# Performance work log

Hardware: AMD Instinct MI355X
Metric: run time of the kernel (lower is better)

The kernel has to match this reference:

```python
import jax, jax.numpy as jnp
import numpy as np

N_LEVELS = 8
BASE_RES = 512
FEAT = 16
N = 1_000_000


def setup_inputs() -> dict:
    key = jax.random.key(0)
    k1, k2, k3 = jax.random.split(key, 3)
    x = jax.random.uniform(k1, (N, 3), dtype=jnp.float32)  # coords in [0,1]^3
    level = jax.random.uniform(k2, (N, 1), dtype=jnp.float32) * (N_LEVELS - 1)
    # texture param: uniform(-0.01, 0.01) as in torch init
    texture = (jax.random.uniform(k3, (3, BASE_RES, BASE_RES, FEAT), dtype=jnp.float32) - 0.5) * 0.02
    return {"x": x, "level": level, "texture": texture}


def _build_mips(texture):
    """Box-filtered mip pyramid: level k has resolution BASE_RES >> k."""
    mips = [texture]
    for _ in range(N_LEVELS - 1):
        t = mips[-1]
        r = t.shape[1]
        t = t.reshape(3, r // 2, 2, r // 2, 2, FEAT).mean(axis=(2, 4))
        mips.append(t)
    return mips


def _bilinear(tex_l, uv):
    """tex_l: (3, r, r, F) [plane, v(row), u(col), feat]; uv: (3, N, 2) in [0,1]. Clamp boundary."""
    r = tex_l.shape[1]
    c = uv * r - 0.5                     # nvdiffrast texel-center convention
    i0f = jnp.floor(c)
    f = c - i0f                          # (3, N, 2) fractional part
    i0 = jnp.clip(i0f.astype(jnp.int32), 0, r - 1)
    i1 = jnp.clip(i0f.astype(jnp.int32) + 1, 0, r - 1)
    u0, v0 = i0[..., 0], i0[..., 1]
    u1, v1 = i1[..., 0], i1[..., 1]
    plane = jnp.arange(3)[:, None]       # (3, 1) broadcast against (3, N)
    t00 = tex_l[plane, v0, u0]           # (3, N, F)
    t01 = tex_l[plane, v0, u1]
    t10 = tex_l[plane, v1, u0]
    t11 = tex_l[plane, v1, u1]
    fu = f[..., 0][..., None]
    fv = f[..., 1][..., None]
    return (t00 * (1 - fu) + t01 * fu) * (1 - fv) + (t10 * (1 - fu) + t11 * fu) * fv


def reference(x, level, texture):
    n = x.shape[0]
    # plane decomposition: uv = (yz, xz, xy), last dim is (u, v)
    uv = jnp.stack([x[:, jnp.array([1, 2])],
                    x[:, jnp.array([0, 2])],
                    x[:, jnp.array([0, 1])]], axis=0)  # (3, N, 2)
    lev = jnp.clip(level[:, 0], 0.0, N_LEVELS - 1)     # (N,)
    l0f = jnp.floor(lev)
    frac = lev - l0f
    l0 = l0f.astype(jnp.int32)
    mips = _build_mips(texture)
    acc = jnp.zeros((3, n, FEAT), dtype=texture.dtype)
    for k in range(N_LEVELS):
        w = jnp.where(l0 == k, 1.0 - frac, 0.0) + jnp.where(l0 + 1 == k, frac, 0.0)  # (N,)
        acc = acc + _bilinear(mips[k], uv) * w[None, :, None]
    # (3, N, F) -> (N, 3, F) -> (N, 3F), matching permute(1,2,0,3).view(N, 3F)
    return acc.transpose(1, 0, 2).reshape(n, 3 * FEAT)
```

## Files before the change

kernel.cpp:

```cpp
#include <hip/hip_runtime.h>
#include <hip/hip_fp16.h>

#define NLEV 8
#define BASE 512

typedef _Float16 h8 __attribute__((ext_vector_type(8)));
typedef float f4v __attribute__((ext_vector_type(4)));
typedef signed char c8 __attribute__((ext_vector_type(8)));

#define QSCALE 12700.0f

__host__ __device__ __forceinline__ long qoff(int k) {
    return (k == 0) ? 0L : (12582912L + 4194304L - (4194304L >> (2 * k - 2)));
}
#define QPYR_BYTES 16776960L
#define QOFF4      16711680L
#define LDSB       65280
__host__ __device__ __forceinline__ long moff(int k) {
    return 4194304L - (4194304L >> (2 * k - 2));
}
#define MIPS_HALVES 4194048L

__global__ __launch_bounds__(256) void ds16_first(const float* __restrict__ src,
                                                  _Float16* __restrict__ dst,
                                                  signed char* __restrict__ qpyr, int r2) {
    int idx = blockIdx.x * blockDim.x + threadIdx.x;
    int total = 3 * r2 * r2 * 2;
    if (idx >= total) return;
    int g = idx & 1;
    int rest = idx >> 1;
    int u = rest % r2; rest /= r2;
    int v = rest % r2;
    int p = rest / r2;
    int rs = r2 * 2;
    const f4v* s4 = (const f4v*)src;
    long t00 = ((long)p * rs + 2 * v) * rs + 2 * u;
    long t01 = t00 + 1, t10 = t00 + rs, t11 = t10 + 1;
    f4v a0 = s4[t00 * 4 + g * 2], a1 = s4[t00 * 4 + g * 2 + 1];
    f4v b0 = s4[t01 * 4 + g * 2], b1 = s4[t01 * 4 + g * 2 + 1];
    f4v c0 = s4[t10 * 4 + g * 2], c1 = s4[t10 * 4 + g * 2 + 1];
    f4v d0 = s4[t11 * 4 + g * 2], d1 = s4[t11 * 4 + g * 2 + 1];
    h8 o;
    c8 qa, qb_, qc, qd, qo;
#pragma unroll
    for (int j = 0; j < 4; ++j) {
        float m0 = (a0[j] + b0[j] + c0[j] + d0[j]) * 0.25f;
        float m1 = (a1[j] + b1[j] + c1[j] + d1[j]) * 0.25f;
        o[j] = (_Float16)m0; o[4 + j] = (_Float16)m1;
        qo[j] = (signed char)(int)rintf(m0 * QSCALE);
        qo[4 + j] = (signed char)(int)rintf(m1 * QSCALE);
        qa[j] = (signed char)(int)rintf(a0[j] * QSCALE); qa[4 + j] = (signed char)(int)rintf(a1[j] * QSCALE);
        qb_[j] = (signed char)(int)rintf(b0[j] * QSCALE); qb_[4 + j] = (signed char)(int)rintf(b1[j] * QSCALE);
        qc[j] = (signed char)(int)rintf(c0[j] * QSCALE); qc[4 + j] = (signed char)(int)rintf(c1[j] * QSCALE);
        qd[j] = (signed char)(int)rintf(d0[j] * QSCALE); qd[4 + j] = (signed char)(int)rintf(d1[j] * QSCALE);
    }
    ((h8*)dst)[idx] = o;
    *(c8*)(qpyr + t00 * 16 + g * 8) = qa;
    *(c8*)(qpyr + t01 * 16 + g * 8) = qb_;
    *(c8*)(qpyr + t10 * 16 + g * 8) = qc;
    *(c8*)(qpyr + t11 * 16 + g * 8) = qd;
    *(c8*)(qpyr + qoff(1) + (long)idx * 8) = qo;
}

__global__ __launch_bounds__(256) void ds16(const _Float16* __restrict__ src,
                                            _Float16* __restrict__ dst,
                                            signed char* __restrict__ qlvl, int r2) {
    int idx = blockIdx.x * blockDim.x + threadIdx.x;
    int total = 3 * r2 * r2 * 2;
    if (idx >= total) return;
    int g = idx & 1;
    int rest = idx >> 1;
    int u = rest % r2; rest /= r2;
    int v = rest % r2;
    int p = rest / r2;
    int rs = r2 * 2;
    const h8* s8 = (const h8*)src;
    long t00 = ((long)p * rs + 2 * v) * rs + 2 * u;
    long t01 = t00 + 1, t10 = t00 + rs, t11 = t10 + 1;
    h8 A = s8[t00 * 2 + g], B = s8[t01 * 2 + g], C = s8[t10 * 2 + g], D = s8[t11 * 2 + g];
    h8 o;
    c8 q;
#pragma unroll
    for (int j = 0; j < 8; ++j) {
        float m = ((float)A[j] + (float)B[j] + (float)C[j] + (float)D[j]) * 0.25f;
        o[j] = (_Float16)m;
        q[j] = (signed char)(int)rintf(m * QSCALE);
    }
    ((h8*)dst)[idx] = o;
    *(c8*)(qlvl + (long)idx * 8) = q;
}

__global__ __launch_bounds__(1024, 2) void tm_sample_l(const float* __restrict__ x,
                                                       const float* __restrict__ level,
                                                       const signed char* __restrict__ qpyr,
                                                       float* __restrict__ out, int n) {
    __shared__ alignas(16) signed char lm[LDSB];
    {
        const f4v* src = (const f4v*)(qpyr + QOFF4);
        f4v* dst = (f4v*)lm;
        for (int idx = threadIdx.x; idx < LDSB / 16; idx += 1024)
            dst[idx] = src[idx];
    }
    __syncthreads();

    int fg = threadIdx.x & 1;
    int usel = (threadIdx.x >> 1) & 1;
    int pid = threadIdx.x >> 2;

    for (long base = (long)blockIdx.x * 256; base < (long)n; base += (long)gridDim.x * 256) {
        int i = (int)(base + pid);
        if (i < n) {
            float px = x[3 * i + 0];
            float py = x[3 * i + 1];
            float pz = x[3 * i + 2];
            float lev = fminf(fmaxf(level[i], 0.0f), (float)(NLEV - 1));
            float l0f = floorf(lev);
            float frac = lev - l0f;
            int l0 = (int)l0f;
            int k1 = min(l0 + 1, NLEV - 1);
            int kk[2] = {l0, k1};

            float uu[3] = {py, px, px};
            float vv[3] = {pz, pz, py};
            const float QINV = 1.0f / QSCALE;
            float lw[2] = {(1.0f - frac) * QINV, frac * QINV};

            c8 tq[12];
            float wgt[12];

#pragma unroll
            for (int s = 0; s < 2; ++s) {
                int k = kk[s];
                int r = BASE >> k;
                float rf = (float)r;
                bool in_lds = (k >= 4);
                long gbase = qoff(k);
                int lbase = (int)(gbase - QOFF4);
#pragma unroll
                for (int p = 0; p < 3; ++p) {
                    float cu = uu[p] * rf - 0.5f;
                    float cv = vv[p] * rf - 0.5f;
                    float fu0 = floorf(cu), fv0 = floorf(cv);
                    float fu = cu - fu0, fv = cv - fv0;
                    int iu0 = (int)fu0, iv0 = (int)fv0;
                    int u0 = min(max(iu0, 0), r - 1);
                    int u1 = min(max(iu0 + 1, 0), r - 1);
                    int v0 = min(max(iv0, 0), r - 1);
                    int v1 = min(max(iv0 + 1, 0), r - 1);
                    int u_ = usel ? u1 : u0;
                    float wu_ = usel ? fu : (1.0f - fu);
                    int pb = p * r * r;
                    int b0 = (pb + v0 * r + u_) * 16 + fg * 8;
                    int b1 = (pb + v1 * r + u_) * 16 + fg * 8;
                    int id = s * 6 + p * 2;
                    if (in_lds) {
                        tq[id + 0] = *(const c8*)(lm + lbase + b0);
                        tq[id + 1] = *(const c8*)(lm + lbase + b1);
                    } else {
                        tq[id + 0] = *(const c8*)(qpyr + gbase + b0);
                        tq[id + 1] = *(const c8*)(qpyr + gbase + b1);
                    }
                    wgt[id + 0] = (1.0f - fv) * wu_ * lw[s];
                    wgt[id + 1] = fv * wu_ * lw[s];
                }
            }

            float acc[3][8];
#pragma unroll
            for (int p = 0; p < 3; ++p)
#pragma unroll
                for (int j = 0; j < 8; ++j) acc[p][j] = 0.f;

#pragma unroll
            for (int s = 0; s < 2; ++s)
#pragma unroll
                for (int p = 0; p < 3; ++p) {
                    int id = s * 6 + p * 2;
                    float w0 = wgt[id + 0], w1 = wgt[id + 1];
#pragma unroll
                    for (int j = 0; j < 8; ++j)
                        acc[p][j] += (float)tq[id + 0][j] * w0 + (float)tq[id + 1][j] * w1;
                }

#pragma unroll
            for (int p = 0; p < 3; ++p)
#pragma unroll
                for (int j = 0; j < 8; ++j)
                    acc[p][j] += __shfl_xor(acc[p][j], 2, 64);

            f4v* o4 = (f4v*)out;
            long ob = (long)i * 12 + fg * 2;
            if (usel == 0) {
                f4v r0 = {acc[0][0], acc[0][1], acc[0][2], acc[0][3]};
                f4v r1 = {acc[0][4], acc[0][5], acc[0][6], acc[0][7]};
                f4v r4 = {acc[2][0], acc[2][1], acc[2][2], acc[2][3]};
                f4v r5 = {acc[2][4], acc[2][5], acc[2][6], acc[2][7]};
                o4[ob + 0] = r0;
                o4[ob + 1] = r1;
                o4[ob + 8] = r4;
                o4[ob + 9] = r5;
            } else {
                f4v r2 = {acc[1][0], acc[1][1], acc[1][2], acc[1][3]};
                f4v r3 = {acc[1][4], acc[1][5], acc[1][6], acc[1][7]};
                o4[ob + 4] = r2;
                o4[ob + 5] = r3;
            }
        }
    }
}

extern "C" void kernel_launch(void* const* d_in, const int* in_sizes, int n_in,
                              void* d_out, int out_size, void* d_ws, size_t ws_size,
                              hipStream_t stream) {
    const float* x     = (const float*)d_in[0];
    const float* level = (const float*)d_in[1];
    const float* tex   = (const float*)d_in[2];
    float* out = (float*)d_out;
    signed char* qpyr = (signed char*)d_ws;
    _Float16* wsh = (_Float16*)((char*)d_ws + QPYR_BYTES);
    int n = in_sizes[0] / 3;

    {
        int r2 = BASE >> 1;
        int total = 3 * r2 * r2 * 2;
        ds16_first<<<(total + 255) / 256, 256, 0, stream>>>(tex, wsh + moff(1), qpyr, r2);
    }
    for (int k = 2; k < NLEV; ++k) {
        int r2 = BASE >> k;
        int total = 3 * r2 * r2 * 2;
        ds16<<<(total + 255) / 256, 256, 0, stream>>>(wsh + moff(k - 1), wsh + moff(k),
                                                      qpyr + qoff(k), r2);
    }

    tm_sample_l<<<512, 1024, 0, stream>>>(x, level, qpyr, out, n);
}
```

Baseline: 141.3 us.

## Split quantized pyramid into feature-half planes and fetch texel pairs with 16-byte loads

The int8 mip pyramid is re-laid out as per-plane, per-feature-half arrays, so two horizontally adjacent texels sit next to each other in 8-byte slots. The sampler now uses two threads per point instead of four. Each thread loads both u-neighbours with a single 16-byte global load and picks the right halves at the clamped boundary, which halves the number of gather instructions and drops the cross-lane shuffle. The LDS staging of the coarse levels is removed, so every level is now read through the cache hierarchy. The twelve loads are issued together through inline asm to increase memory-level parallelism, at the cost of more registers per thread.

```diff
diff --git a/kernel.cpp b/kernel.cpp
--- a/kernel.cpp
+++ b/kernel.cpp
@@ -7,6 +7,8 @@
 typedef _Float16 h8 __attribute__((ext_vector_type(8)));
 typedef float f4v __attribute__((ext_vector_type(4)));
 typedef signed char c8 __attribute__((ext_vector_type(8)));
+typedef signed char c16 __attribute__((ext_vector_type(16)));
+typedef int  i4v __attribute__((ext_vector_type(4)));
 
 #define QSCALE 12700.0f
 
@@ -14,8 +16,6 @@
     return (k == 0) ? 0L : (12582912L + 4194304L - (4194304L >> (2 * k - 2)));
 }
 #define QPYR_BYTES 16776960L
-#define QOFF4      16711680L
-#define LDSB       65280
 __host__ __device__ __forceinline__ long moff(int k) {
     return 4194304L - (4194304L >> (2 * k - 2));
 }
@@ -49,17 +49,19 @@
         o[j] = (_Float16)m0; o[4 + j] = (_Float16)m1;
         qo[j] = (signed char)(int)rintf(m0 * QSCALE);
         qo[4 + j] = (signed char)(int)rintf(m1 * QSCALE);
-        qa[j] = (signed char)(int)rintf(a0[j] * QSCALE); qa[4 + j] = (signed char)(int)rintf(a1[j] * QSCALE);
+        qa[j] = (signed char)(int)rintf(a0[j] * QSCALE);  qa[4 + j] = (signed char)(int)rintf(a1[j] * QSCALE);
         qb_[j] = (signed char)(int)rintf(b0[j] * QSCALE); qb_[4 + j] = (signed char)(int)rintf(b1[j] * QSCALE);
-        qc[j] = (signed char)(int)rintf(c0[j] * QSCALE); qc[4 + j] = (signed char)(int)rintf(c1[j] * QSCALE);
-        qd[j] = (signed char)(int)rintf(d0[j] * QSCALE); qd[4 + j] = (signed char)(int)rintf(d1[j] * QSCALE);
+        qc[j] = (signed char)(int)rintf(c0[j] * QSCALE);  qc[4 + j] = (signed char)(int)rintf(c1[j] * QSCALE);
+        qd[j] = (signed char)(int)rintf(d0[j] * QSCALE);  qd[4 + j] = (signed char)(int)rintf(d1[j] * QSCALE);
     }
     ((h8*)dst)[idx] = o;
-    *(c8*)(qpyr + t00 * 16 + g * 8) = qa;
-    *(c8*)(qpyr + t01 * 16 + g * 8) = qb_;
-    *(c8*)(qpyr + t10 * 16 + g * 8) = qc;
-    *(c8*)(qpyr + t11 * 16 + g * 8) = qd;
-    *(c8*)(qpyr + qoff(1) + (long)idx * 8) = qo;
+    long ph = (long)(p * 2 + g) * 262144;
+    long w00 = (long)(2 * v) * 512 + 2 * u;
+    c16 Q0 = __builtin_shufflevector(qa, qb_, 0,1,2,3,4,5,6,7,8,9,10,11,12,13,14,15);
+    c16 Q1 = __builtin_shufflevector(qc, qd, 0,1,2,3,4,5,6,7,8,9,10,11,12,13,14,15);
+    *(c16*)(qpyr + (ph + w00) * 8) = Q0;
+    *(c16*)(qpyr + (ph + w00 + 512) * 8) = Q1;
+    *(c8*)(qpyr + qoff(1) + ((long)(p * 2 + g) * 65536 + (long)v * 256 + u) * 8) = qo;
 }
 
 __global__ __launch_bounds__(256) void ds16(const _Float16* __restrict__ src,
@@ -87,125 +89,113 @@
         q[j] = (signed char)(int)rintf(m * QSCALE);
     }
     ((h8*)dst)[idx] = o;
-    *(c8*)(qlvl + (long)idx * 8) = q;
-}
-
-__global__ __launch_bounds__(1024, 2) void tm_sample_l(const float* __restrict__ x,
-                                                       const float* __restrict__ level,
-                                                       const signed char* __restrict__ qpyr,
-                                                       float* __restrict__ out, int n) {
-    __shared__ alignas(16) signed char lm[LDSB];
-    {
-        const f4v* src = (const f4v*)(qpyr + QOFF4);
-        f4v* dst = (f4v*)lm;
-        for (int idx = threadIdx.x; idx < LDSB / 16; idx += 1024)
-            dst[idx] = src[idx];
-    }
-    __syncthreads();
-
-    int fg = threadIdx.x & 1;
-    int usel = (threadIdx.x >> 1) & 1;
-    int pid = threadIdx.x >> 2;
-
-    for (long base = (long)blockIdx.x * 256; base < (long)n; base += (long)gridDim.x * 256) {
-        int i = (int)(base + pid);
-        if (i < n) {
-            float px = x[3 * i + 0];
-            float py = x[3 * i + 1];
-            float pz = x[3 * i + 2];
-            float lev = fminf(fmaxf(level[i], 0.0f), (float)(NLEV - 1));
-            float l0f = floorf(lev);
-            float frac = lev - l0f;
-            int l0 = (int)l0f;
-            int k1 = min(l0 + 1, NLEV - 1);
-            int kk[2] = {l0, k1};
-
-            float uu[3] = {py, px, px};
-            float vv[3] = {pz, pz, py};
-            const float QINV = 1.0f / QSCALE;
-            float lw[2] = {(1.0f - frac) * QINV, frac * QINV};
-
-            c8 tq[12];
-            float wgt[12];
-
-#pragma unroll
-            for (int s = 0; s < 2; ++s) {
-                int k = kk[s];
-                int r = BASE >> k;
-                float rf = (float)r;
-                bool in_lds = (k >= 4);
-                long gbase = qoff(k);
-                int lbase = (int)(gbase - QOFF4);
-#pragma unroll
-                for (int p = 0; p < 3; ++p) {
-                    float cu = uu[p] * rf - 0.5f;
-                    float cv = vv[p] * rf - 0.5f;
-                    float fu0 = floorf(cu), fv0 = floorf(cv);
-                    float fu = cu - fu0, fv = cv - fv0;
-                    int iu0 = (int)fu0, iv0 = (int)fv0;
-                    int u0 = min(max(iu0, 0), r - 1);
-                    int u1 = min(max(iu0 + 1, 0), r - 1);
-                    int v0 = min(max(iv0, 0), r - 1);
-                    int v1 = min(max(iv0 + 1, 0), r - 1);
-                    int u_ = usel ? u1 : u0;
-                    float wu_ = usel ? fu : (1.0f - fu);
-                    int pb = p * r * r;
-                    int b0 = (pb + v0 * r + u_) * 16 + fg * 8;
-                    int b1 = (pb + v1 * r + u_) * 16 + fg * 8;
-                    int id = s * 6 + p * 2;
-                    if (in_lds) {
-                        tq[id + 0] = *(const c8*)(lm + lbase + b0);
-                        tq[id + 1] = *(const c8*)(lm + lbase + b1);
-                    } else {
-                        tq[id + 0] = *(const c8*)(qpyr + gbase + b0);
-                        tq[id + 1] = *(const c8*)(qpyr + gbase + b1);
-                    }
-                    wgt[id + 0] = (1.0f - fv) * wu_ * lw[s];
-                    wgt[id + 1] = fv * wu_ * lw[s];
-                }
-            }
-
-            float acc[3][8];
-#pragma unroll
-            for (int p = 0; p < 3; ++p)
-#pragma unroll
-                for (int j = 0; j < 8; ++j) acc[p][j] = 0.f;
-
-#pragma unroll
-            for (int s = 0; s < 2; ++s)
-#pragma unroll
-                for (int p = 0; p < 3; ++p) {
-                    int id = s * 6 + p * 2;
-                    float w0 = wgt[id + 0], w1 = wgt[id + 1];
-#pragma unroll
-                    for (int j = 0; j < 8; ++j)
-                        acc[p][j] += (float)tq[id + 0][j] * w0 + (float)tq[id + 1][j] * w1;
-                }
-
-#pragma unroll
-            for (int p = 0; p < 3; ++p)
-#pragma unroll
-                for (int j = 0; j < 8; ++j)
-                    acc[p][j] += __shfl_xor(acc[p][j], 2, 64);
-
-            f4v* o4 = (f4v*)out;
-            long ob = (long)i * 12 + fg * 2;
-            if (usel == 0) {
-                f4v r0 = {acc[0][0], acc[0][1], acc[0][2], acc[0][3]};
-                f4v r1 = {acc[0][4], acc[0][5], acc[0][6], acc[0][7]};
-                f4v r4 = {acc[2][0], acc[2][1], acc[2][2], acc[2][3]};
-                f4v r5 = {acc[2][4], acc[2][5], acc[2][6], acc[2][7]};
-                o4[ob + 0] = r0;
-                o4[ob + 1] = r1;
-                o4[ob + 8] = r4;
-                o4[ob + 9] = r5;
-            } else {
-                f4v r2 = {acc[1][0], acc[1][1], acc[1][2], acc[1][3]};
-                f4v r3 = {acc[1][4], acc[1][5], acc[1][6], acc[1][7]};
-                o4[ob + 4] = r2;
-                o4[ob + 5] = r3;
-            }
+    *(c8*)(qlvl + ((long)(p * 2 + g) * r2 * r2 + (long)v * r2 + u) * 8) = q;
+}
+
+__global__ __launch_bounds__(256) void tm_sample2(const float* __restrict__ x,
+                                                  const float* __restrict__ level,
+                                                  const signed char* __restrict__ qpyr,
+                                                  float* __restrict__ out, int n) {
+    int t = blockIdx.x * blockDim.x + threadIdx.x;
+    int i = t >> 1;
+    if (i >= n) return;
+    int fg = t & 1;
+
+    float px = x[3 * i + 0];
+    float py = x[3 * i + 1];
+    float pz = x[3 * i + 2];
+    float lev = fminf(fmaxf(level[i], 0.0f), (float)(NLEV - 1));
+    float l0f = floorf(lev);
+    float frac = lev - l0f;
+    int l0 = (int)l0f;
+    int k1 = min(l0 + 1, NLEV - 1);
+    int kk[2] = {l0, k1};
+
+    float uu[3] = {py, px, px};
+    float vv[3] = {pz, pz, py};
+    const float QINV = 1.0f / QSCALE;
+    float lw[2] = {(1.0f - frac) * QINV, frac * QINV};
+
+    const signed char* ap[12];
+    float wgt[24];
+    bool sA[6], sB[6];
+
+#pragma unroll
+    for (int s = 0; s < 2; ++s) {
+        int k = kk[s];
+        int r = BASE >> k;
+        float rf = (float)r;
+        long lvl = qoff(k);
+#pragma unroll
+        for (int p = 0; p < 3; ++p) {
+            int id = s * 3 + p;
+            float cu = uu[p] * rf - 0.5f;
+            float cv = vv[p] * rf - 0.5f;
+            float fu0 = floorf(cu), fv0 = floorf(cv);
+            float fu = cu - fu0, fv = cv - fv0;
+            int iu0 = (int)fu0, iv0 = (int)fv0;
+            int v0 = min(max(iv0, 0), r - 1);
+            int v1 = min(max(iv0 + 1, 0), r - 1);
+            int ub = min(max(iu0, 0), r - 2);
+            sA[id] = (iu0 >= r - 1);
+            sB[id] = (iu0 >= 0);
+            const signed char* bp = qpyr + lvl + ((long)(p * 2 + fg) * r * r + ub) * 8;
+            ap[id * 2 + 0] = bp + (long)v0 * r * 8;
+            ap[id * 2 + 1] = bp + (long)v1 * r * 8;
+            float w = lw[s];
+            wgt[id * 4 + 0] = (1.0f - fu) * (1.0f - fv) * w;
+            wgt[id * 4 + 1] = fu * (1.0f - fv) * w;
+            wgt[id * 4 + 2] = (1.0f - fu) * fv * w;
+            wgt[id * 4 + 3] = fu * fv * w;
         }
+    }
+
+    i4v d[12];
+#pragma unroll
+    for (int m = 0; m < 12; ++m)
+        asm volatile("global_load_dwordx4 %0, %1, off"
+                     : "=v"(d[m]) : "v"(ap[m]) : "memory");
+    asm volatile("s_waitcnt vmcnt(0)"
+                 : "+v"(d[0]), "+v"(d[1]), "+v"(d[2]), "+v"(d[3]),
+                   "+v"(d[4]), "+v"(d[5]), "+v"(d[6]), "+v"(d[7]),
+                   "+v"(d[8]), "+v"(d[9]), "+v"(d[10]), "+v"(d[11])
+                 :: "memory");
+
+    float acc[3][8];
+#pragma unroll
+    for (int p = 0; p < 3; ++p)
+#pragma unroll
+        for (int j = 0; j < 8; ++j) acc[p][j] = 0.f;
+
+#pragma unroll
+    for (int id = 0; id < 6; ++id) {
+        int p = id % 3;
+        c16 r0 = __builtin_bit_cast(c16, d[id * 2 + 0]);
+        c16 r1 = __builtin_bit_cast(c16, d[id * 2 + 1]);
+        c8 lo0 = __builtin_shufflevector(r0, r0, 0,1,2,3,4,5,6,7);
+        c8 hi0 = __builtin_shufflevector(r0, r0, 8,9,10,11,12,13,14,15);
+        c8 lo1 = __builtin_shufflevector(r1, r1, 0,1,2,3,4,5,6,7);
+        c8 hi1 = __builtin_shufflevector(r1, r1, 8,9,10,11,12,13,14,15);
+        c8 A = sA[id] ? hi0 : lo0;
+        c8 B = sB[id] ? hi0 : lo0;
+        c8 C = sA[id] ? hi1 : lo1;
+        c8 D = sB[id] ? hi1 : lo1;
+        float w00 = wgt[id * 4 + 0], w01 = wgt[id * 4 + 1];
+        float w10 = wgt[id * 4 + 2], w11 = wgt[id * 4 + 3];
+#pragma unroll
+        for (int j = 0; j < 8; ++j)
+            acc[p][j] += (float)A[j] * w00 + (float)B[j] * w01
+                       + (float)C[j] * w10 + (float)D[j] * w11;
+    }
+
+    f4v* o4 = (f4v*)out;
+    long ob = (long)i * 12 + fg * 2;
+#pragma unroll
+    for (int p = 0; p < 3; ++p) {
+        f4v r0 = {acc[p][0], acc[p][1], acc[p][2], acc[p][3]};
+        f4v r1 = {acc[p][4], acc[p][5], acc[p][6], acc[p][7]};
+        o4[ob + p * 4 + 0] = r0;
+        o4[ob + p * 4 + 1] = r1;
     }
 }
 
@@ -232,5 +222,7 @@
                                                       qpyr + qoff(k), r2);
     }
 
-    tm_sample_l<<<512, 1024, 0, stream>>>(x, level, qpyr, out, n);
-}
+    long tt = (long)n * 2;
+    int blocks = (int)((tt + 255) / 256);
+    tm_sample2<<<blocks, 256, 0, stream>>>(x, level, qpyr, out, n);
+}
```

Result: slower. 171.0 us (+21.1%).

## Fuse coarse mip levels into one kernel and drop LDS staging in sampler

Applied to the files above, without the earlier changes.

Builds mip levels 4-7 in a single kernel that keeps intermediate levels in shared memory, replacing four small launches with one. The sampler no longer copies the coarse int8 levels into LDS. It now uses one thread per quarter-point with a flat grid instead of a persistent grid-stride loop, and writes output with uniform nontemporal stores. This cuts launch overhead and the per-block LDS fill cost, but coarse-level lookups now go through global memory and cache instead of LDS.

```diff
diff --git a/kernel.cpp b/kernel.cpp
--- a/kernel.cpp
+++ b/kernel.cpp
@@ -14,12 +14,9 @@
     return (k == 0) ? 0L : (12582912L + 4194304L - (4194304L >> (2 * k - 2)));
 }
 #define QPYR_BYTES 16776960L
-#define QOFF4      16711680L
-#define LDSB       65280
 __host__ __device__ __forceinline__ long moff(int k) {
     return 4194304L - (4194304L >> (2 * k - 2));
 }
-#define MIPS_HALVES 4194048L
 
 __global__ __launch_bounds__(256) void ds16_first(const float* __restrict__ src,
                                                   _Float16* __restrict__ dst,
@@ -49,10 +46,10 @@
         o[j] = (_Float16)m0; o[4 + j] = (_Float16)m1;
         qo[j] = (signed char)(int)rintf(m0 * QSCALE);
         qo[4 + j] = (signed char)(int)rintf(m1 * QSCALE);
-        qa[j] = (signed char)(int)rintf(a0[j] * QSCALE); qa[4 + j] = (signed char)(int)rintf(a1[j] * QSCALE);
+        qa[j] = (signed char)(int)rintf(a0[j] * QSCALE);  qa[4 + j] = (signed char)(int)rintf(a1[j] * QSCALE);
         qb_[j] = (signed char)(int)rintf(b0[j] * QSCALE); qb_[4 + j] = (signed char)(int)rintf(b1[j] * QSCALE);
-        qc[j] = (signed char)(int)rintf(c0[j] * QSCALE); qc[4 + j] = (signed char)(int)rintf(c1[j] * QSCALE);
-        qd[j] = (signed char)(int)rintf(d0[j] * QSCALE); qd[4 + j] = (signed char)(int)rintf(d1[j] * QSCALE);
+        qc[j] = (signed char)(int)rintf(c0[j] * QSCALE);  qc[4 + j] = (signed char)(int)rintf(c1[j] * QSCALE);
+        qd[j] = (signed char)(int)rintf(d0[j] * QSCALE);  qd[4 + j] = (signed char)(int)rintf(d1[j] * QSCALE);
     }
     ((h8*)dst)[idx] = o;
     *(c8*)(qpyr + t00 * 16 + g * 8) = qa;
@@ -90,122 +87,162 @@
     *(c8*)(qlvl + (long)idx * 8) = q;
 }
 
-__global__ __launch_bounds__(1024, 2) void tm_sample_l(const float* __restrict__ x,
-                                                       const float* __restrict__ level,
-                                                       const signed char* __restrict__ qpyr,
-                                                       float* __restrict__ out, int n) {
-    __shared__ alignas(16) signed char lm[LDSB];
+__global__ __launch_bounds__(1024) void ds_rest(const _Float16* __restrict__ m3,
+                                                signed char* __restrict__ qpyr) {
+    __shared__ h8 l4[1024];
+    __shared__ h8 l5[256];
+    __shared__ h8 l6[64];
+    int p = blockIdx.x >> 1, g = blockIdx.x & 1;
+    int t = threadIdx.x;
+    const h8* s8 = (const h8*)m3;
+
     {
-        const f4v* src = (const f4v*)(qpyr + QOFF4);
-        f4v* dst = (f4v*)lm;
-        for (int idx = threadIdx.x; idx < LDSB / 16; idx += 1024)
-            dst[idx] = src[idx];
+        int v = t >> 5, u = t & 31;
+        long t00 = ((long)p * 64 + 2 * v) * 64 + 2 * u;
+        h8 A = s8[t00 * 2 + g], B = s8[(t00 + 1) * 2 + g];
+        h8 C = s8[(t00 + 64) * 2 + g], D = s8[(t00 + 65) * 2 + g];
+        h8 o; c8 q;
+#pragma unroll
+        for (int j = 0; j < 8; ++j) {
+            float m = ((float)A[j] + (float)B[j] + (float)C[j] + (float)D[j]) * 0.25f;
+            o[j] = (_Float16)m;
+            q[j] = (signed char)(int)rintf(m * QSCALE);
+        }
+        l4[v * 32 + u] = o;
+        *(c8*)(qpyr + qoff(4) + (((long)(p * 32 + v) * 32 + u) * 2 + g) * 8) = q;
     }
     __syncthreads();
-
-    int fg = threadIdx.x & 1;
-    int usel = (threadIdx.x >> 1) & 1;
-    int pid = threadIdx.x >> 2;
-
-    for (long base = (long)blockIdx.x * 256; base < (long)n; base += (long)gridDim.x * 256) {
-        int i = (int)(base + pid);
-        if (i < n) {
-            float px = x[3 * i + 0];
-            float py = x[3 * i + 1];
-            float pz = x[3 * i + 2];
-            float lev = fminf(fmaxf(level[i], 0.0f), (float)(NLEV - 1));
-            float l0f = floorf(lev);
-            float frac = lev - l0f;
-            int l0 = (int)l0f;
-            int k1 = min(l0 + 1, NLEV - 1);
-            int kk[2] = {l0, k1};
-
-            float uu[3] = {py, px, px};
-            float vv[3] = {pz, pz, py};
-            const float QINV = 1.0f / QSCALE;
-            float lw[2] = {(1.0f - frac) * QINV, frac * QINV};
-
-            c8 tq[12];
-            float wgt[12];
-
-#pragma unroll
-            for (int s = 0; s < 2; ++s) {
-                int k = kk[s];
-                int r = BASE >> k;
-                float rf = (float)r;
-                bool in_lds = (k >= 4);
-                long gbase = qoff(k);
-                int lbase = (int)(gbase - QOFF4);
-#pragma unroll
-                for (int p = 0; p < 3; ++p) {
-                    float cu = uu[p] * rf - 0.5f;
-                    float cv = vv[p] * rf - 0.5f;
-                    float fu0 = floorf(cu), fv0 = floorf(cv);
-                    float fu = cu - fu0, fv = cv - fv0;
-                    int iu0 = (int)fu0, iv0 = (int)fv0;
-                    int u0 = min(max(iu0, 0), r - 1);
-                    int u1 = min(max(iu0 + 1, 0), r - 1);
-                    int v0 = min(max(iv0, 0), r - 1);
-                    int v1 = min(max(iv0 + 1, 0), r - 1);
-                    int u_ = usel ? u1 : u0;
-                    float wu_ = usel ? fu : (1.0f - fu);
-                    int pb = p * r * r;
-                    int b0 = (pb + v0 * r + u_) * 16 + fg * 8;
-                    int b1 = (pb + v1 * r + u_) * 16 + fg * 8;
-                    int id = s * 6 + p * 2;
-                    if (in_lds) {
-                        tq[id + 0] = *(const c8*)(lm + lbase + b0);
-                        tq[id + 1] = *(const c8*)(lm + lbase + b1);
-                    } else {
-                        tq[id + 0] = *(const c8*)(qpyr + gbase + b0);
-                        tq[id + 1] = *(const c8*)(qpyr + gbase + b1);
-                    }
-                    wgt[id + 0] = (1.0f - fv) * wu_ * lw[s];
-                    wgt[id + 1] = fv * wu_ * lw[s];
-                }
-            }
-
-            float acc[3][8];
-#pragma unroll
-            for (int p = 0; p < 3; ++p)
-#pragma unroll
-                for (int j = 0; j < 8; ++j) acc[p][j] = 0.f;
-
-#pragma unroll
-            for (int s = 0; s < 2; ++s)
-#pragma unroll
-                for (int p = 0; p < 3; ++p) {
-                    int id = s * 6 + p * 2;
-                    float w0 = wgt[id + 0], w1 = wgt[id + 1];
-#pragma unroll
-                    for (int j = 0; j < 8; ++j)
-                        acc[p][j] += (float)tq[id + 0][j] * w0 + (float)tq[id + 1][j] * w1;
-                }
-
-#pragma unroll
-            for (int p = 0; p < 3; ++p)
-#pragma unroll
-                for (int j = 0; j < 8; ++j)
-                    acc[p][j] += __shfl_xor(acc[p][j], 2, 64);
-
-            f4v* o4 = (f4v*)out;
-            long ob = (long)i * 12 + fg * 2;
-            if (usel == 0) {
-                f4v r0 = {acc[0][0], acc[0][1], acc[0][2], acc[0][3]};
-                f4v r1 = {acc[0][4], acc[0][5], acc[0][6], acc[0][7]};
-                f4v r4 = {acc[2][0], acc[2][1], acc[2][2], acc[2][3]};
-                f4v r5 = {acc[2][4], acc[2][5], acc[2][6], acc[2][7]};
-                o4[ob + 0] = r0;
-                o4[ob + 1] = r1;
-                o4[ob + 8] = r4;
-                o4[ob + 9] = r5;
-            } else {
-                f4v r2 = {acc[1][0], acc[1][1], acc[1][2], acc[1][3]};
-                f4v r3 = {acc[1][4], acc[1][5], acc[1][6], acc[1][7]};
-                o4[ob + 4] = r2;
-                o4[ob + 5] = r3;
-            }
-        }
+    if (t < 256) {
+        int v = t >> 4, u = t & 15;
+        h8 A = l4[(2 * v) * 32 + 2 * u], B = l4[(2 * v) * 32 + 2 * u + 1];
+        h8 C = l4[(2 * v + 1) * 32 + 2 * u], D = l4[(2 * v + 1) * 32 + 2 * u + 1];
+        h8 o; c8 q;
+#pragma unroll
+        for (int j = 0; j < 8; ++j) {
+            float m = ((float)A[j] + (float)B[j] + (float)C[j] + (float)D[j]) * 0.25f;
+            o[j] = (_Float16)m;
+            q[j] = (signed char)(int)rintf(m * QSCALE);
+        }
+        l5[v * 16 + u] = o;
+        *(c8*)(qpyr + qoff(5) + (((long)(p * 16 + v) * 16 + u) * 2 + g) * 8) = q;
+    }
+    __syncthreads();
+    if (t < 64) {
+        int v = t >> 3, u = t & 7;
+        h8 A = l5[(2 * v) * 16 + 2 * u], B = l5[(2 * v) * 16 + 2 * u + 1];
+        h8 C = l5[(2 * v + 1) * 16 + 2 * u], D = l5[(2 * v + 1) * 16 + 2 * u + 1];
+        h8 o; c8 q;
+#pragma unroll
+        for (int j = 0; j < 8; ++j) {
+            float m = ((float)A[j] + (float)B[j] + (float)C[j] + (float)D[j]) * 0.25f;
+            o[j] = (_Float16)m;
+            q[j] = (signed char)(int)rintf(m * QSCALE);
+        }
+        l6[v * 8 + u] = o;
+        *(c8*)(qpyr + qoff(6) + (((long)(p * 8 + v) * 8 + u) * 2 + g) * 8) = q;
+    }
+    __syncthreads();
+    if (t < 16) {
+        int v = t >> 2, u = t & 3;
+        h8 A = l6[(2 * v) * 8 + 2 * u], B = l6[(2 * v) * 8 + 2 * u + 1];
+        h8 C = l6[(2 * v + 1) * 8 + 2 * u], D = l6[(2 * v + 1) * 8 + 2 * u + 1];
+        c8 q;
+#pragma unroll
+        for (int j = 0; j < 8; ++j) {
+            float m = ((float)A[j] + (float)B[j] + (float)C[j] + (float)D[j]) * 0.25f;
+            q[j] = (signed char)(int)rintf(m * QSCALE);
+        }
+        *(c8*)(qpyr + qoff(7) + (((long)(p * 4 + v) * 4 + u) * 2 + g) * 8) = q;
+    }
+}
+
+__global__ __launch_bounds__(256) void tm_sample_q(const float* __restrict__ x,
+                                                   const float* __restrict__ level,
+                                                   const signed char* __restrict__ qpyr,
+                                                   float* __restrict__ out, int n) {
+    int t = blockIdx.x * blockDim.x + threadIdx.x;
+    int i = t >> 2;
+    if (i >= n) return;
+    int fg = t & 1;
+    int usel = (t >> 1) & 1;
+
+    float px = x[3 * i + 0];
+    float py = x[3 * i + 1];
+    float pz = x[3 * i + 2];
+    float lev = fminf(fmaxf(level[i], 0.0f), (float)(NLEV - 1));
+    float l0f = floorf(lev);
+    float frac = lev - l0f;
+    int l0 = (int)l0f;
+    int k1 = min(l0 + 1, NLEV - 1);
+
+    float uu[3] = {py, px, px};
+    float vv[3] = {pz, pz, py};
+    int rr[2] = {BASE >> l0, BASE >> k1};
+    const signed char* qb[2] = {qpyr + qoff(l0), qpyr + qoff(k1)};
+    const float QINV = 1.0f / QSCALE;
+    float lw[2] = {(1.0f - frac) * QINV, frac * QINV};
+
+    c8 tq[12];
+    float wgt[12];
+
+#pragma unroll
+    for (int s = 0; s < 2; ++s) {
+        int r = rr[s];
+        float rf = (float)r;
+#pragma unroll
+        for (int p = 0; p < 3; ++p) {
+            float cu = uu[p] * rf - 0.5f;
+            float cv = vv[p] * rf - 0.5f;
+            float fu0 = floorf(cu), fv0 = floorf(cv);
+            float fu = cu - fu0, fv = cv - fv0;
+            int iu0 = (int)fu0, iv0 = (int)fv0;
+            int u0 = min(max(iu0, 0), r - 1);
+            int u1 = min(max(iu0 + 1, 0), r - 1);
+            int v0 = min(max(iv0, 0), r - 1);
+            int v1 = min(max(iv0 + 1, 0), r - 1);
+            int u_ = usel ? u1 : u0;
+            float wu_ = usel ? fu : (1.0f - fu);
+            long pb = (long)p * r * r;
+            long b0 = (pb + (long)v0 * r + u_) * 16 + fg * 8;
+            long b1 = (pb + (long)v1 * r + u_) * 16 + fg * 8;
+            int id = s * 6 + p * 2;
+            tq[id + 0] = *(const c8*)(qb[s] + b0);
+            tq[id + 1] = *(const c8*)(qb[s] + b1);
+            wgt[id + 0] = (1.0f - fv) * wu_ * lw[s];
+            wgt[id + 1] = fv * wu_ * lw[s];
+        }
+    }
+
+    float acc[3][8];
+#pragma unroll
+    for (int p = 0; p < 3; ++p)
+#pragma unroll
+        for (int j = 0; j < 8; ++j) acc[p][j] = 0.f;
+
+#pragma unroll
+    for (int s = 0; s < 2; ++s)
+#pragma unroll
+        for (int p = 0; p < 3; ++p) {
+            int id = s * 6 + p * 2;
+            float w0 = wgt[id + 0], w1 = wgt[id + 1];
+#pragma unroll
+            for (int j = 0; j < 8; ++j)
+                acc[p][j] += (float)tq[id + 0][j] * w0 + (float)tq[id + 1][j] * w1;
+        }
+
+#pragma unroll
+    for (int p = 0; p < 3; ++p)
+#pragma unroll
+        for (int j = 0; j < 8; ++j)
+            acc[p][j] += __shfl_xor(acc[p][j], 2, 64);
+
+    f4v* o4 = (f4v*)out;
+    long ob = (long)i * 12 + fg * 2 + usel;
+#pragma unroll
+    for (int p = 0; p < 3; ++p) {
+        f4v r0 = {acc[p][usel * 4 + 0], acc[p][usel * 4 + 1],
+                  acc[p][usel * 4 + 2], acc[p][usel * 4 + 3]};
+        __builtin_nontemporal_store(r0, &o4[ob + p * 4]);
     }
 }
 
@@ -225,12 +262,15 @@
         int total = 3 * r2 * r2 * 2;
         ds16_first<<<(total + 255) / 256, 256, 0, stream>>>(tex, wsh + moff(1), qpyr, r2);
     }
-    for (int k = 2; k < NLEV; ++k) {
+    for (int k = 2; k <= 3; ++k) {
         int r2 = BASE >> k;
         int total = 3 * r2 * r2 * 2;
         ds16<<<(total + 255) / 256, 256, 0, stream>>>(wsh + moff(k - 1), wsh + moff(k),
                                                       qpyr + qoff(k), r2);
     }
-
-    tm_sample_l<<<512, 1024, 0, stream>>>(x, level, qpyr, out, n);
-}
+    ds_rest<<<6, 1024, 0, stream>>>(wsh + moff(3), qpyr);
+
+    long tt = (long)n * 4;
+    int blocks = (int)((tt + 255) / 256);
+    tm_sample_q<<<blocks, 256, 0, stream>>>(x, level, qpyr, out, n);
+}
```

After: 192.4 us. 1.36x slower.
